# Optimization experiments

Hardware: AMD Instinct MI355X
Metric: run time of the kernel (lower is better)

Reference implementation:

```python
import jax, jax.numpy as jnp
import numpy as np

DIM = 128
EPS = 1e-5

def _layernorm(x, w, b, eps=EPS):
    mu = jnp.mean(x, axis=-1, keepdims=True)
    var = jnp.mean(jnp.square(x - mu), axis=-1, keepdims=True)
    return (x - mu) * jax.lax.rsqrt(var + eps) * w + b

def setup_inputs() -> dict:
    key = jax.random.key(0)
    ks = jax.random.split(key, 6)
    B, N, D = 1, 512, DIM
    x = jax.random.normal(ks[0], (B, N, N, D), dtype=jnp.float32)
    mask = jnp.ones((B, N, N), dtype=jnp.float32)
    # parameters (torch Linear weight is [out, in]; we store [in, out] for x @ W)
    lecun = 1.0 / np.sqrt(D)
    w_p_in = jax.random.normal(ks[1], (D, 2 * D), dtype=jnp.float32) * lecun
    w_g_in = jnp.zeros((D, 2 * D), dtype=jnp.float32)   # gating_init -> zeros
    w_p_out = jnp.zeros((D, D), dtype=jnp.float32)      # final_init -> zeros
    w_g_out = jnp.zeros((D, D), dtype=jnp.float32)      # gating_init -> zeros
    # use small random values instead of exact zeros to make the math non-trivial
    w_g_in = jax.random.normal(ks[2], (D, 2 * D), dtype=jnp.float32) * 0.02
    w_p_out = jax.random.normal(ks[3], (D, D), dtype=jnp.float32) * 0.02
    w_g_out = jax.random.normal(ks[4], (D, D), dtype=jnp.float32) * 0.02
    norm_in_w = jnp.ones((D,), jnp.float32)
    norm_in_b = jnp.zeros((D,), jnp.float32)
    norm_out_w = jnp.ones((D,), jnp.float32)
    norm_out_b = jnp.zeros((D,), jnp.float32)
    return {
        "x": x, "mask": mask,
        "w_p_in": w_p_in, "w_g_in": w_g_in,
        "w_p_out": w_p_out, "w_g_out": w_g_out,
        "norm_in_w": norm_in_w, "norm_in_b": norm_in_b,
        "norm_out_w": norm_out_w, "norm_out_b": norm_out_b,
    }

def reference(x, mask, w_p_in, w_g_in, w_p_out, w_g_out,
              norm_in_w, norm_in_b, norm_out_w, norm_out_b):
    # x: [B,N,N,D], mask: [B,N,N]
    xn = _layernorm(x, norm_in_w, norm_in_b)          # norm_in
    x_in = xn
    p = xn @ w_p_in                                   # [B,N,N,2D]
    g = jax.nn.sigmoid(xn @ w_g_in)
    h = p * g * mask[..., None]                       # gated + masked
    a, b = jnp.split(h.astype(jnp.float32), 2, axis=-1)  # each [B,N,N,D]
    t = jnp.einsum('bikd,bjkd->bijd', a, b)           # triangular matmul
    tn = _layernorm(t, norm_out_w, norm_out_b)        # norm_out (eps=1e-5)
    out = (tn @ w_p_out) * jax.nn.sigmoid(x_in @ w_g_out)
    return out
```

## Files before the change

kernel.cpp:

```cpp
#include <hip/hip_runtime.h>
#include <hip/hip_bf16.h>
#include <math.h>

#define NN 512
#define DD 128
#define NP (NN*NN)

#define PITCH ((size_t)(NP * 2 + 256))

typedef __attribute__((ext_vector_type(4))) float f32x4;
typedef __attribute__((ext_vector_type(8))) short bf16x8;

__device__ __forceinline__ unsigned short f2bf(float f) {
  union { float f; unsigned u; } v; v.f = f;
  unsigned r = v.u + 0x7FFFu + ((v.u >> 16) & 1u);
  return (unsigned short)(r >> 16);
}
__device__ __forceinline__ float bf2f(unsigned short h) {
  union { unsigned u; float f; } v; v.u = ((unsigned)h) << 16;
  return v.f;
}
__device__ __forceinline__ float sigmoidf_(float x) {
  return __builtin_amdgcn_rcpf(1.0f + __expf(-x));
}
__device__ __forceinline__ unsigned pkbf2(float a, float b) {
  float2 t; t.x = a; t.y = b;
  __hip_bfloat162 h = __float22bfloat162_rn(t);
  unsigned r; __builtin_memcpy(&r, &h, 4); return r;
}

__device__ __forceinline__ void gll16(void* lds, const void* g) {
  __builtin_amdgcn_global_load_lds(
      (const __attribute__((address_space(1))) void*)g,
      (__attribute__((address_space(3))) void*)lds, 16, 0, 0);
}

#define WP_P  0
#define WP_G  65536
#define WP_GO 131072
#define WP_PO 163840

__global__ __launch_bounds__(256) void kw_prep(const float* __restrict__ w_p_in,
    const float* __restrict__ w_g_in, const float* __restrict__ w_g_out,
    const float* __restrict__ w_p_out, unsigned short* __restrict__ wprep) {
  int idx = blockIdx.x * 256 + threadIdx.x;
  int n, k, base; float v;
  if (idx < 32768)       { n = idx >> 7;          k = idx & 127; v = w_p_in[k * 256 + n];  base = WP_P; }
  else if (idx < 65536)  { int e = idx - 32768;  n = e >> 7; k = e & 127; v = w_g_in[k * 256 + n];  base = WP_G; }
  else if (idx < 81920)  { int e = idx - 65536;  n = e >> 7; k = e & 127; v = w_g_out[k * 128 + n]; base = WP_GO; }
  else                   { int e = idx - 81920;  n = e >> 7; k = e & 127; v = w_p_out[k * 128 + n]; base = WP_PO; }
  int dst = base + n * 256 + ((2 * k) ^ ((n & 7) << 4));
  wprep[dst >> 1] = f2bf(v);
}

__global__ __launch_bounds__(256) void kAB(
    const float* __restrict__ x, const float* __restrict__ mask,
    const unsigned short* __restrict__ wprep,
    const float* __restrict__ nw, const float* __restrict__ nb,
    unsigned short* __restrict__ xn_sw,
    unsigned char* __restrict__ a_t, unsigned char* __restrict__ b_t) {
  const int row0 = blockIdx.x * 128;
  const int tid = threadIdx.x, lane = tid & 63, wv = tid >> 6;
  const int wr = wv >> 1, wc = wv & 1;
  __shared__ __align__(16) unsigned char sxn[32768];
  __shared__ __align__(16) unsigned char sepi[16384];
  __shared__ float smask[128];

  const int l16 = tid & 15, rsub = tid >> 4;
  if (tid < 128) smask[tid] = mask[row0 + tid];
  const float4 wv0 = *(const float4*)(nw + l16 * 8);
  const float4 wv1 = *(const float4*)(nw + l16 * 8 + 4);
  const float4 bv0 = *(const float4*)(nb + l16 * 8);
  const float4 bv1 = *(const float4*)(nb + l16 * 8 + 4);
  #pragma unroll
  for (int rnd = 0; rnd < 8; ++rnd) {
    int r = rnd * 16 + rsub;
    const float* xr = x + (size_t)(row0 + r) * DD + l16 * 8;
    float4 v0 = *(const float4*)xr;
    float4 v1 = *(const float4*)(xr + 4);
    float s = v0.x + v0.y + v0.z + v0.w + v1.x + v1.y + v1.z + v1.w;
    float q = v0.x*v0.x + v0.y*v0.y + v0.z*v0.z + v0.w*v0.w
            + v1.x*v1.x + v1.y*v1.y + v1.z*v1.z + v1.w*v1.w;
    #pragma unroll
    for (int m = 8; m; m >>= 1) { s += __shfl_xor(s, m); q += __shfl_xor(q, m); }
    float mean = s * (1.0f / DD);
    float var = q * (1.0f / DD) - mean * mean;
    float rstd = rsqrtf(var + 1e-5f);
    uint4 pk;
    pk.x = pkbf2((v0.x - mean) * rstd * wv0.x + bv0.x, (v0.y - mean) * rstd * wv0.y + bv0.y);
    pk.y = pkbf2((v0.z - mean) * rstd * wv0.z + bv0.z, (v0.w - mean) * rstd * wv0.w + bv0.w);
    pk.z = pkbf2((v1.x - mean) * rstd * wv1.x + bv1.x, (v1.y - mean) * rstd * wv1.y + bv1.y);
    pk.w = pkbf2((v1.z - mean) * rstd * wv1.z + bv1.z, (v1.w - mean) * rstd * wv1.w + bv1.w);
    int off = ((l16 * 16) ^ ((r & 7) << 4));
    *(uint4*)(sxn + r * 256 + off) = pk;
    *(uint4*)((unsigned char*)xn_sw + (size_t)(row0 + r) * 256 + off) = pk;
  }
  __syncthreads();

  const unsigned char* wp = (const unsigned char*)wprep;

  for (int q = 0; q < 4; ++q) {
    f32x4 acc[4][4] = {};
    #pragma unroll
    for (int ks = 0; ks < 4; ++ks) {
      int kb = ks * 64 + (lane >> 4) * 16;
      bf16x8 af[4], bfr[4];
      #pragma unroll
      for (int mi = 0; mi < 4; ++mi) {
        int r = wr * 64 + mi * 16 + (lane & 15);
        af[mi] = *(const bf16x8*)(sxn + r * 256 + (kb ^ ((r & 7) << 4)));
      }
      #pragma unroll
      for (int ni = 0; ni < 2; ++ni) {
        int n = q * 64 + wc * 32 + ni * 16 + (lane & 15);
        int off = n * 256 + (kb ^ ((n & 7) << 4));
        bfr[ni]     = *(const bf16x8*)(wp + WP_P + off);
        bfr[ni + 2] = *(const bf16x8*)(wp + WP_G + off);
      }
      #pragma unroll
      for (int mi = 0; mi < 4; ++mi)
        #pragma unroll
        for (int ni = 0; ni < 4; ++ni)
          acc[mi][ni] = __builtin_amdgcn_mfma_f32_16x16x32_bf16(af[mi], bfr[ni], acc[mi][ni], 0, 0, 0);
    }
    #pragma unroll
    for (int mi = 0; mi < 4; ++mi) {
      int rq = wr * 64 + mi * 16 + (lane >> 4) * 4;
      float mk0 = smask[rq], mk1 = smask[rq + 1], mk2 = smask[rq + 2], mk3 = smask[rq + 3];
      #pragma unroll
      for (int ni = 0; ni < 2; ++ni) {
        int drel = wc * 32 + ni * 16 + (lane & 15);
        uint2 pk;
        pk.x = pkbf2(acc[mi][ni][0] * sigmoidf_(acc[mi][ni + 2][0]) * mk0,
                     acc[mi][ni][1] * sigmoidf_(acc[mi][ni + 2][1]) * mk1);
        pk.y = pkbf2(acc[mi][ni][2] * sigmoidf_(acc[mi][ni + 2][2]) * mk2,
                     acc[mi][ni][3] * sigmoidf_(acc[mi][ni + 2][3]) * mk3);
        *(uint2*)(sepi + drel * 256 + ((rq * 2) ^ ((drel & 7) << 4))) = pk;
      }
    }
    __syncthreads();
    unsigned char* dst = (q < 2) ? a_t : b_t;
    const int dmin = (q & 1) * 64;
    #pragma unroll
    for (int it = 0; it < 4; ++it) {
      int idx = it * 256 + tid;
      int dr = idx >> 4, ch = idx & 15;
      uint4 v = *(const uint4*)(sepi + dr * 256 + ((ch * 16) ^ ((dr & 7) << 4)));
      *(uint4*)(dst + (size_t)(dmin + dr) * PITCH + (size_t)(row0 + ch * 8) * 2) = v;
    }
    __syncthreads();
  }
}

__global__ __launch_bounds__(256) void k2_einsum(
    const unsigned char* __restrict__ a_t, const unsigned char* __restrict__ b_t,
    unsigned char* __restrict__ t_out) {
  int bid = blockIdx.x;
  int wg = (bid & 7) * 256 + (bid >> 3);
  int d = wg >> 4;
  int tile = wg & 15;
  int i0 = (tile >> 2) * 128, j0 = (tile & 3) * 128;
  const int tid = threadIdx.x, lane = tid & 63, wv = tid >> 6;
  const int wr = wv >> 1, wc = wv & 1;
  __shared__ __align__(16) unsigned char smem[32768];
  unsigned char* sA0 = smem;
  unsigned char* sB0 = smem + 16384;
  const unsigned char* Abase = a_t + (size_t)d * PITCH + (size_t)i0 * 1024;
  const unsigned char* Bbase = b_t + (size_t)d * PITCH + (size_t)j0 * 1024;

  const int so0 = tid * 16;
  const int r0s = so0 >> 6, c0s = (so0 >> 4) & 3;
  const size_t ga0 = (size_t)r0s * 1024 + ((c0s ^ ((r0s >> 1) & 3)) << 4);
  const int so1 = so0 + 4096;
  const int r1s = so1 >> 6, c1s = (so1 >> 4) & 3;
  const size_t ga1 = (size_t)r1s * 1024 + ((c1s ^ ((r1s >> 1) & 3)) << 4);

  f32x4 acc[4][4] = {};
  gll16(sA0 + so0, Abase + ga0);
  gll16(sB0 + so0, Bbase + ga0);
  gll16(sA0 + so1, Abase + ga1);
  gll16(sB0 + so1, Bbase + ga1);
  __syncthreads();

  int cur = 0;
  for (int t = 0; t < 16; ++t) {
    if (t < 15) {
      int nk = (t + 1) * 64;
      int nb_ = (cur ^ 1) * 8192;
      gll16(sA0 + nb_ + so0, Abase + ga0 + nk);
      gll16(sB0 + nb_ + so0, Bbase + ga0 + nk);
      gll16(sA0 + nb_ + so1, Abase + ga1 + nk);
      gll16(sB0 + nb_ + so1, Bbase + ga1 + nk);
    }
    bf16x8 af[4], bfr[4];
    const int kc = lane >> 4;
    int cb = cur * 8192;
    #pragma unroll
    for (int mi = 0; mi < 4; ++mi) {
      int r = wr * 64 + mi * 16 + (lane & 15);
      af[mi] = *(const bf16x8*)(sA0 + cb + r * 64 + ((kc ^ ((r >> 1) & 3)) << 4));
    }
    #pragma unroll
    for (int ni = 0; ni < 4; ++ni) {
      int r = wc * 64 + ni * 16 + (lane & 15);
      bfr[ni] = *(const bf16x8*)(sB0 + cb + r * 64 + ((kc ^ ((r >> 1) & 3)) << 4));
    }
    #pragma unroll
    for (int mi = 0; mi < 4; ++mi)
      #pragma unroll
      for (int ni = 0; ni < 4; ++ni)
        acc[mi][ni] = __builtin_amdgcn_mfma_f32_16x16x32_bf16(af[mi], bfr[ni], acc[mi][ni], 0, 0, 0);
    __syncthreads();
    cur ^= 1;
  }

  #pragma unroll
  for (int mi = 0; mi < 4; ++mi)
    #pragma unroll
    for (int j = 0; j < 4; ++j) {
      int il = wr * 64 + mi * 16 + (lane >> 4) * 4 + j;
      #pragma unroll
      for (int ni = 0; ni < 4; ++ni) {
        int jl = wc * 64 + ni * 16 + (lane & 15);
        *(unsigned short*)(smem + il * 256 + ((jl * 2) ^ ((il & 7) << 4))) = f2bf(acc[mi][ni][j]);
      }
    }
  __syncthreads();
  unsigned char* trow = t_out + (size_t)d * PITCH;
  #pragma unroll
  for (int rr = 0; rr < 8; ++rr) {
    int idx = rr * 256 + tid;
    int il = idx >> 4, ch = idx & 15;
    uint4 v = *(const uint4*)(smem + il * 256 + ((ch * 16) ^ ((il & 7) << 4)));
    *(uint4*)(trow + (size_t)(i0 + il) * 1024 + (size_t)(j0 + ch * 8) * 2) = v;
  }
}

__global__ __launch_bounds__(256) void k3_out(
    const unsigned char* __restrict__ t_in, const unsigned short* __restrict__ xn_sw,
    const unsigned short* __restrict__ wprep,
    const float* __restrict__ now, const float* __restrict__ nob,
    float* __restrict__ out) {
  const int p0 = blockIdx.x * 64;
  const int tid = threadIdx.x, lane = tid & 63, wv = tid >> 6;
  const int wr = wv >> 1, wc = wv & 1;
  __shared__ __align__(16) unsigned char sm[49152];
  unsigned short* sT = (unsigned short*)sm;
  unsigned char* sTN = sm + 16384;
  unsigned char* sxn = sm + 32768;
  __shared__ float ps[4][64], pq[4][64], smean[64], srstd[64];

  #pragma unroll
  for (int it = 0; it < 4; ++it) {
    int o = it * 4096 + tid * 16;
    int dr = o >> 7, cb = o & 127;
    gll16((unsigned char*)sT + o, t_in + (size_t)dr * PITCH + (size_t)p0 * 2 + cb);
  }
  #pragma unroll
  for (int it = 0; it < 4; ++it) {
    int o = it * 4096 + tid * 16;
    gll16(sxn + o, (const unsigned char*)xn_sw + (size_t)p0 * 256 + o);
  }
  __syncthreads();
  const int p = tid & 63, dh = tid >> 6;
  {
    float s = 0.f, q = 0.f;
    #pragma unroll
    for (int dd = 0; dd < 32; ++dd) {
      float v = bf2f(sT[(dh * 32 + dd) * 64 + p]);
      s += v; q += v * v;
    }
    ps[dh][p] = s; pq[dh][p] = q;
  }
  __syncthreads();
  if (tid < 64) {
    float s = ps[0][tid] + ps[1][tid] + ps[2][tid] + ps[3][tid];
    float q = pq[0][tid] + pq[1][tid] + pq[2][tid] + pq[3][tid];
    float mean = s * (1.0f / 128.0f);
    float var = q * (1.0f / 128.0f) - mean * mean;
    smean[tid] = mean; srstd[tid] = rsqrtf(var + 1e-5f);
  }
  __syncthreads();
  {
    float mean = smean[p], rstd = srstd[p];
    #pragma unroll
    for (int e = 0; e < 16; ++e) {
      int d0 = dh * 32 + e * 2;
      float v0 = (bf2f(sT[d0 * 64 + p]) - mean) * rstd * now[d0] + nob[d0];
      float v1 = (bf2f(sT[(d0 + 1) * 64 + p]) - mean) * rstd * now[d0 + 1] + nob[d0 + 1];
      unsigned pack = pkbf2(v0, v1);
      *(unsigned*)(sTN + p * 256 + ((d0 * 2) ^ ((p & 7) << 4))) = pack;
    }
  }
  __syncthreads();
  f32x4 accP[2][4] = {}, accG[2][4] = {};
  const unsigned char* wpo = (const unsigned char*)wprep + WP_PO;
  const unsigned char* wgo = (const unsigned char*)wprep + WP_GO;
  #pragma unroll
  for (int ks = 0; ks < 4; ++ks) {
    int kb = ks * 64 + (lane >> 4) * 16;
    bf16x8 af[2], ag[2], bP[4], bG[4];
    #pragma unroll
    for (int mi = 0; mi < 2; ++mi) {
      int r = wr * 32 + mi * 16 + (lane & 15);
      int off = r * 256 + (kb ^ ((r & 7) << 4));
      af[mi] = *(const bf16x8*)(sTN + off);
      ag[mi] = *(const bf16x8*)(sxn + off);
    }
    #pragma unroll
    for (int ni = 0; ni < 4; ++ni) {
      int n = wc * 64 + ni * 16 + (lane & 15);
      int off = n * 256 + (kb ^ ((n & 7) << 4));
      bP[ni] = *(const bf16x8*)(wpo + off);
      bG[ni] = *(const bf16x8*)(wgo + off);
    }
    #pragma unroll
    for (int mi = 0; mi < 2; ++mi)
      #pragma unroll
      for (int ni = 0; ni < 4; ++ni) {
        accP[mi][ni] = __builtin_amdgcn_mfma_f32_16x16x32_bf16(af[mi], bP[ni], accP[mi][ni], 0, 0, 0);
        accG[mi][ni] = __builtin_amdgcn_mfma_f32_16x16x32_bf16(ag[mi], bG[ni], accG[mi][ni], 0, 0, 0);
      }
  }
  __syncthreads();
  #pragma unroll
  for (int mi = 0; mi < 2; ++mi)
    #pragma unroll
    for (int ni = 0; ni < 4; ++ni) {
      int nb4 = (wc * 256 + ni * 64 + (lane & 15) * 4);
      int prow = wr * 32 + mi * 16 + (lane >> 4) * 4;
      #pragma unroll
      for (int j = 0; j < 4; ++j) {
        int pp = prow + j;
        float v = accP[mi][ni][j] * sigmoidf_(accG[mi][ni][j]);
        *(float*)(sm + pp * 512 + (nb4 ^ (((pp >> 2) & 3) << 6))) = v;
      }
    }
  __syncthreads();
  #pragma unroll
  for (int it = 0; it < 8; ++it) {
    int idx = it * 256 + tid;
    int pp = idx >> 5, ch = idx & 31;
    uint4 v = *(const uint4*)(sm + pp * 512 + ((ch * 16) ^ (((pp >> 2) & 3) << 6)));
    *(uint4*)((unsigned char*)out + (size_t)(p0 + pp) * 512 + ch * 16) = v;
  }
}

extern "C" void kernel_launch(void* const* d_in, const int* in_sizes, int n_in,
                              void* d_out, int out_size, void* d_ws, size_t ws_size,
                              hipStream_t stream) {
  (void)in_sizes; (void)n_in; (void)out_size; (void)ws_size;
  const float* x         = (const float*)d_in[0];
  const float* mask      = (const float*)d_in[1];
  const float* w_p_in    = (const float*)d_in[2];
  const float* w_g_in    = (const float*)d_in[3];
  const float* w_p_out   = (const float*)d_in[4];
  const float* w_g_out   = (const float*)d_in[5];
  const float* norm_in_w = (const float*)d_in[6];
  const float* norm_in_b = (const float*)d_in[7];
  const float* norm_out_w= (const float*)d_in[8];
  const float* norm_out_b= (const float*)d_in[9];
  float* out = (float*)d_out;

  unsigned char* ws = (unsigned char*)d_ws;
  const size_t SLAB = (size_t)128 * PITCH;
  unsigned char* a_t    = ws;
  unsigned char* b_t    = ws + SLAB;
  unsigned char* t_buf  = ws + 2 * SLAB;
  unsigned short* xn_sw = (unsigned short*)(ws + 3 * SLAB);
  unsigned short* wprep = (unsigned short*)(ws + 3 * SLAB + (size_t)NP * 256);

  kw_prep<<<384, 256, 0, stream>>>(w_p_in, w_g_in, w_g_out, w_p_out, wprep);
  kAB<<<2048, 256, 0, stream>>>(x, mask, wprep, norm_in_w, norm_in_b, xn_sw, a_t, b_t);
  k2_einsum<<<2048, 256, 0, stream>>>(a_t, b_t, t_buf);
  k3_out<<<4096, 256, 0, stream>>>(t_buf, xn_sw, wprep, norm_out_w, norm_out_b, out);
}
```

Baseline: 246.6 us.

## Retile intermediate a/b/t layouts into blocked chunks for contiguous einsum and output loads

The a/b intermediates are now written in a blocked layout (k-chunks of 128 by i-row of 256 bytes), so the einsum kernel loads contiguous 256-byte rows with a 128-wide k step. It uses double-buffered 32KB tiles and half as many iterations. The t output is stored as 64-pixel blocks of all d channels, so k3 reads one contiguous 16KB span instead of strided per-channel rows. Shared memory grows to 64KB in the einsum kernel, which may lower occupancy.

```diff
diff --git a/kernel.cpp b/kernel.cpp
--- a/kernel.cpp
+++ b/kernel.cpp
@@ -60,6 +60,8 @@
     unsigned short* __restrict__ xn_sw,
     unsigned char* __restrict__ a_t, unsigned char* __restrict__ b_t) {
   const int row0 = blockIdx.x * 128;
+  const int i_idx = row0 >> 9;
+  const int kb = (row0 & 511) >> 7;
   const int tid = threadIdx.x, lane = tid & 63, wv = tid >> 6;
   const int wr = wv >> 1, wc = wv & 1;
   __shared__ __align__(16) unsigned char sxn[32768];
@@ -103,17 +105,17 @@
     f32x4 acc[4][4] = {};
     #pragma unroll
     for (int ks = 0; ks < 4; ++ks) {
-      int kb = ks * 64 + (lane >> 4) * 16;
+      int kbb = ks * 64 + (lane >> 4) * 16;
       bf16x8 af[4], bfr[4];
       #pragma unroll
       for (int mi = 0; mi < 4; ++mi) {
         int r = wr * 64 + mi * 16 + (lane & 15);
-        af[mi] = *(const bf16x8*)(sxn + r * 256 + (kb ^ ((r & 7) << 4)));
+        af[mi] = *(const bf16x8*)(sxn + r * 256 + (kbb ^ ((r & 7) << 4)));
       }
       #pragma unroll
       for (int ni = 0; ni < 2; ++ni) {
         int n = q * 64 + wc * 32 + ni * 16 + (lane & 15);
-        int off = n * 256 + (kb ^ ((n & 7) << 4));
+        int off = n * 256 + (kbb ^ ((n & 7) << 4));
         bfr[ni]     = *(const bf16x8*)(wp + WP_P + off);
         bfr[ni + 2] = *(const bf16x8*)(wp + WP_G + off);
       }
@@ -146,7 +148,8 @@
       int idx = it * 256 + tid;
       int dr = idx >> 4, ch = idx & 15;
       uint4 v = *(const uint4*)(sepi + dr * 256 + ((ch * 16) ^ ((dr & 7) << 4)));
-      *(uint4*)(dst + (size_t)(dmin + dr) * PITCH + (size_t)(row0 + ch * 8) * 2) = v;
+      *(uint4*)(dst + (size_t)(dmin + dr) * PITCH + (size_t)kb * 131072
+                    + (size_t)i_idx * 256 + ch * 16) = v;
     }
     __syncthreads();
   }
@@ -162,54 +165,62 @@
   int i0 = (tile >> 2) * 128, j0 = (tile & 3) * 128;
   const int tid = threadIdx.x, lane = tid & 63, wv = tid >> 6;
   const int wr = wv >> 1, wc = wv & 1;
-  __shared__ __align__(16) unsigned char smem[32768];
-  unsigned char* sA0 = smem;
-  unsigned char* sB0 = smem + 16384;
-  const unsigned char* Abase = a_t + (size_t)d * PITCH + (size_t)i0 * 1024;
-  const unsigned char* Bbase = b_t + (size_t)d * PITCH + (size_t)j0 * 1024;
-
-  const int so0 = tid * 16;
-  const int r0s = so0 >> 6, c0s = (so0 >> 4) & 3;
-  const size_t ga0 = (size_t)r0s * 1024 + ((c0s ^ ((r0s >> 1) & 3)) << 4);
-  const int so1 = so0 + 4096;
-  const int r1s = so1 >> 6, c1s = (so1 >> 4) & 3;
-  const size_t ga1 = (size_t)r1s * 1024 + ((c1s ^ ((r1s >> 1) & 3)) << 4);
+  __shared__ __align__(16) unsigned char smem[65536];
+  unsigned char* sA = smem;
+  unsigned char* sB = smem + 32768;
+  const unsigned char* Abase = a_t + (size_t)d * PITCH;
+  const unsigned char* Bbase = b_t + (size_t)d * PITCH;
+
+  int sil[4], sga[4];
+  #pragma unroll
+  for (int j = 0; j < 4; ++j) {
+    int o = j * 4096 + tid * 16;
+    int il = o >> 7, c = (o >> 4) & 7;
+    sil[j] = o;
+    sga[j] = il * 256 + ((c ^ (il & 7)) << 4);
+  }
 
   f32x4 acc[4][4] = {};
-  gll16(sA0 + so0, Abase + ga0);
-  gll16(sB0 + so0, Bbase + ga0);
-  gll16(sA0 + so1, Abase + ga1);
-  gll16(sB0 + so1, Bbase + ga1);
+  #pragma unroll
+  for (int j = 0; j < 4; ++j) {
+    gll16(sA + sil[j], Abase + (size_t)(i0) * 256 + sga[j]);
+    gll16(sB + sil[j], Bbase + (size_t)(j0) * 256 + sga[j]);
+  }
   __syncthreads();
 
   int cur = 0;
-  for (int t = 0; t < 16; ++t) {
-    if (t < 15) {
-      int nk = (t + 1) * 64;
-      int nb_ = (cur ^ 1) * 8192;
-      gll16(sA0 + nb_ + so0, Abase + ga0 + nk);
-      gll16(sB0 + nb_ + so0, Bbase + ga0 + nk);
-      gll16(sA0 + nb_ + so1, Abase + ga1 + nk);
-      gll16(sB0 + nb_ + so1, Bbase + ga1 + nk);
-    }
-    bf16x8 af[4], bfr[4];
-    const int kc = lane >> 4;
-    int cb = cur * 8192;
-    #pragma unroll
-    for (int mi = 0; mi < 4; ++mi) {
-      int r = wr * 64 + mi * 16 + (lane & 15);
-      af[mi] = *(const bf16x8*)(sA0 + cb + r * 64 + ((kc ^ ((r >> 1) & 3)) << 4));
-    }
-    #pragma unroll
-    for (int ni = 0; ni < 4; ++ni) {
-      int r = wc * 64 + ni * 16 + (lane & 15);
-      bfr[ni] = *(const bf16x8*)(sB0 + cb + r * 64 + ((kc ^ ((r >> 1) & 3)) << 4));
-    }
-    #pragma unroll
-    for (int mi = 0; mi < 4; ++mi)
-      #pragma unroll
-      for (int ni = 0; ni < 4; ++ni)
-        acc[mi][ni] = __builtin_amdgcn_mfma_f32_16x16x32_bf16(af[mi], bfr[ni], acc[mi][ni], 0, 0, 0);
+  for (int t = 0; t < 8; ++t) {
+    if (t < 7) {
+      int tn = t + 1;
+      size_t koff = (size_t)(tn >> 1) * 131072 + (size_t)(tn & 1) * 128;
+      int nb_ = (cur ^ 1) * 16384;
+      #pragma unroll
+      for (int j = 0; j < 4; ++j) {
+        gll16(sA + nb_ + sil[j], Abase + koff + (size_t)i0 * 256 + sga[j]);
+        gll16(sB + nb_ + sil[j], Bbase + koff + (size_t)j0 * 256 + sga[j]);
+      }
+    }
+    int cb = cur * 16384;
+    #pragma unroll
+    for (int ks2 = 0; ks2 < 2; ++ks2) {
+      bf16x8 af[4], bfr[4];
+      int cfrag = ks2 * 4 + (lane >> 4);
+      #pragma unroll
+      for (int mi = 0; mi < 4; ++mi) {
+        int r = wr * 64 + mi * 16 + (lane & 15);
+        af[mi] = *(const bf16x8*)(sA + cb + r * 128 + ((cfrag ^ (r & 7)) << 4));
+      }
+      #pragma unroll
+      for (int ni = 0; ni < 4; ++ni) {
+        int r = wc * 64 + ni * 16 + (lane & 15);
+        bfr[ni] = *(const bf16x8*)(sB + cb + r * 128 + ((cfrag ^ (r & 7)) << 4));
+      }
+      #pragma unroll
+      for (int mi = 0; mi < 4; ++mi)
+        #pragma unroll
+        for (int ni = 0; ni < 4; ++ni)
+          acc[mi][ni] = __builtin_amdgcn_mfma_f32_16x16x32_bf16(af[mi], bfr[ni], acc[mi][ni], 0, 0, 0);
+    }
     __syncthreads();
     cur ^= 1;
   }
@@ -226,13 +237,14 @@
       }
     }
   __syncthreads();
-  unsigned char* trow = t_out + (size_t)d * PITCH;
   #pragma unroll
   for (int rr = 0; rr < 8; ++rr) {
-    int idx = rr * 256 + tid;
-    int il = idx >> 4, ch = idx & 15;
-    uint4 v = *(const uint4*)(smem + il * 256 + ((ch * 16) ^ ((il & 7) << 4)));
-    *(uint4*)(trow + (size_t)(i0 + il) * 1024 + (size_t)(j0 + ch * 8) * 2) = v;
+    int u = rr * 256 + tid;
+    int il = u >> 4, sub = u & 15;
+    int jg = sub >> 3, cc = sub & 7;
+    uint4 v = *(const uint4*)(smem + il * 256 + ((sub * 16) ^ ((il & 7) << 4)));
+    *(uint4*)(t_out + ((size_t)(i0 + il) * 8 + (j0 >> 6) + jg) * 16384
+                    + (size_t)d * 128 + cc * 16) = v;
   }
 }
 
@@ -253,8 +265,7 @@
   #pragma unroll
   for (int it = 0; it < 4; ++it) {
     int o = it * 4096 + tid * 16;
-    int dr = o >> 7, cb = o & 127;
-    gll16((unsigned char*)sT + o, t_in + (size_t)dr * PITCH + (size_t)p0 * 2 + cb);
+    gll16((unsigned char*)sT + o, t_in + (size_t)blockIdx.x * 16384 + o);
   }
   #pragma unroll
   for (int it = 0; it < 4; ++it) {
@@ -298,19 +309,19 @@
   const unsigned char* wgo = (const unsigned char*)wprep + WP_GO;
   #pragma unroll
   for (int ks = 0; ks < 4; ++ks) {
-    int kb = ks * 64 + (lane >> 4) * 16;
+    int kbb = ks * 64 + (lane >> 4) * 16;
     bf16x8 af[2], ag[2], bP[4], bG[4];
     #pragma unroll
     for (int mi = 0; mi < 2; ++mi) {
       int r = wr * 32 + mi * 16 + (lane & 15);
-      int off = r * 256 + (kb ^ ((r & 7) << 4));
+      int off = r * 256 + (kbb ^ ((r & 7) << 4));
       af[mi] = *(const bf16x8*)(sTN + off);
       ag[mi] = *(const bf16x8*)(sxn + off);
     }
     #pragma unroll
     for (int ni = 0; ni < 4; ++ni) {
       int n = wc * 64 + ni * 16 + (lane & 15);
-      int off = n * 256 + (kb ^ ((n & 7) << 4));
+      int off = n * 256 + (kbb ^ ((n & 7) << 4));
       bP[ni] = *(const bf16x8*)(wpo + off);
       bG[ni] = *(const bf16x8*)(wgo + off);
     }
```

After: 243.3 us. No clear change (-1.3%).
